# Optimization experiments

Measured on AMD Instinct MI355X. Metric: run time of the kernel, lower is better.

The kernel has to match this reference:

```python
import jax, jax.numpy as jnp
import numpy as np
import math

WINDOW_SIZE = 11
DATA_RANGE = 1.0
SIGMA = 1.5


def _gaussian_window(C):
    xs = np.arange(WINDOW_SIZE)
    g = np.exp(-((xs - WINDOW_SIZE // 2) ** 2) / (2.0 * SIGMA ** 2))
    g = (g / g.sum()).astype(np.float32)
    w2d = np.outer(g, g)  # [K,K]
    # depthwise kernel: [C, 1, K, K] in OIHW with feature_group_count=C
    w = np.broadcast_to(w2d, (C, 1, WINDOW_SIZE, WINDOW_SIZE))
    return jnp.asarray(w)


def _dwconv(x, w, C):
    pad = WINDOW_SIZE // 2
    return jax.lax.conv_general_dilated(
        x, w, window_strides=(1, 1), padding=((pad, pad), (pad, pad)),
        dimension_numbers=('NCHW', 'OIHW', 'NCHW'), feature_group_count=C)


def setup_inputs() -> dict:
    key = jax.random.key(0)
    k1, k2 = jax.random.split(key)
    B, C, H, W = 16, 3, 512, 512
    img1 = jax.random.uniform(k1, (B, C, H, W), dtype=jnp.float32)
    img2 = jax.random.uniform(k2, (B, C, H, W), dtype=jnp.float32)
    return {"img1": img1, "img2": img2}


def reference(img1, img2):
    C = img1.shape[1]
    w = _gaussian_window(C)
    C1 = (0.01 * DATA_RANGE) ** 2
    C2 = (0.03 * DATA_RANGE) ** 2

    mu1 = _dwconv(img1, w, C)
    mu2 = _dwconv(img2, w, C)
    mu1_sq = mu1 * mu1
    mu2_sq = mu2 * mu2
    mu1_mu2 = mu1 * mu2
    sigma1_sq = _dwconv(img1 * img1, w, C) - mu1_sq
    sigma2_sq = _dwconv(img2 * img2, w, C) - mu2_sq
    sigma12 = _dwconv(img1 * img2, w, C) - mu1_mu2

    ssim_map = ((2 * mu1_mu2 + C1) * (2 * sigma12 + C2)) / (
        (mu1_sq + mu2_sq + C1) * (sigma1_sq + sigma2_sq + C2))
    ssim_val = ssim_map.mean(axis=(1, 2, 3)).mean()  # size_average=True
    return 1.0 - ssim_val
```

## Files before the change

kernel.cpp:

```cpp
#include <hip/hip_runtime.h>
#include <math.h>

typedef float v2f __attribute__((ext_vector_type(2)));

#define TILE 32
#define HALO 5
#define IN_T 42
#define ROWP 42
#define SINT_P 33
#define HWDIM 512
#define NPLANES 48
#define NBLK (16*16*48)
#define NPIX (16ull*3ull*512ull*512ull)

struct GW { float g[11]; };

__global__ __launch_bounds__(256) void ssim_reduce(
    const float* __restrict__ partial, float* __restrict__ out)
{
    __shared__ float s_red[4];
    const int tid = threadIdx.x;
    float s = 0.0f;
#pragma unroll
    for (int k = 0; k < NBLK / 256; ++k) s += partial[tid + k * 256];
#pragma unroll
    for (int off = 32; off > 0; off >>= 1) s += __shfl_down(s, off, 64);
    if ((tid & 63) == 0) s_red[tid >> 6] = s;
    __syncthreads();
    if (tid == 0) {
        const float tot = s_red[0] + s_red[1] + s_red[2] + s_red[3];
        out[0] = 1.0f - tot * (1.0f / (float)NPIX);
    }
}

__global__ __launch_bounds__(256, 4) void ssim_main(
    const float* __restrict__ img1, const float* __restrict__ img2,
    float* __restrict__ partial, GW gw)
{
    __shared__ alignas(16) v2f sxy[IN_T][ROWP];
    __shared__ alignas(16) float4 s_int[IN_T][SINT_P];
    __shared__ float s_red[4];

    const int tid = threadIdx.x;
    const int tx = blockIdx.x, ty = blockIdx.y, plane = blockIdx.z;
    const float* __restrict__ p1 = img1 + (size_t)plane * (HWDIM * HWDIM);
    const float* __restrict__ p2 = img2 + (size_t)plane * (HWDIM * HWDIM);
    const int gy0 = ty * TILE - HALO;
    const int gx0 = tx * TILE - HALO;

    for (int idx = tid; idx < IN_T * ROWP; idx += 256) {
        const int r = idx / ROWP;
        const int c = idx - r * ROWP;
        const int gy = gy0 + r, gx = gx0 + c;
        float a = 0.0f, b = 0.0f;
        if (gy >= 0 && gy < HWDIM && gx >= 0 && gx < HWDIM) {
            const int off = gy * HWDIM + gx;
            a = p1[off];
            b = p2[off];
        }
        v2f pr; pr.x = a; pr.y = b;
        sxy[r][c] = pr;
    }
    __syncthreads();

    for (int item = tid; item < IN_T * 8; item += 256) {
        const int g8 = item / IN_T;
        const int r  = item - g8 * IN_T;
        const int c0 = g8 * 4;

        v2f xy[14];
#pragma unroll
        for (int j = 0; j < 7; ++j) {
            const float4 f = *reinterpret_cast<const float4*>(&sxy[r][c0 + 2 * j]);
            v2f t0; t0.x = f.x; t0.y = f.y;
            v2f t1; t1.x = f.z; t1.y = f.w;
            xy[2 * j]     = t0;
            xy[2 * j + 1] = t1;
        }

        v2f accA[4], accB[4];
#pragma unroll
        for (int o = 0; o < 4; ++o) { accA[o] = 0.0f; accB[o] = 0.0f; }

#pragma unroll
        for (int e = 0; e < 14; ++e) {
            const v2f p = xy[e];
            const float u = p.x + p.y;
            const float w = p.x - p.y;
            v2f uv; uv.x = u; uv.y = w;
            const v2f qq = uv * uv;
#pragma unroll
            for (int o = 0; o < 4; ++o) {
                const int k = e - o;
                if (k >= 0 && k < 11) {
                    v2f gg; gg.x = gw.g[k]; gg.y = gw.g[k];
                    accA[o] = __builtin_elementwise_fma(gg, p,  accA[o]);
                    accB[o] = __builtin_elementwise_fma(gg, qq, accB[o]);
                }
            }
        }
#pragma unroll
        for (int o = 0; o < 4; ++o)
            s_int[r][c0 + o] = make_float4(accA[o].x, accA[o].y, accB[o].x, accB[o].y);
    }
    __syncthreads();

    const int c  = tid & 31;
    const int r0 = (tid >> 5) * 4;
    v2f vA[4], vB[4];
#pragma unroll
    for (int o = 0; o < 4; ++o) { vA[o] = 0.0f; vB[o] = 0.0f; }

#pragma unroll
    for (int j = 0; j < 14; ++j) {
        const float4 f = s_int[r0 + j][c];
        v2f A; A.x = f.x; A.y = f.y;
        v2f B; B.x = f.z; B.y = f.w;
#pragma unroll
        for (int o = 0; o < 4; ++o) {
            const int k = j - o;
            if (k >= 0 && k < 11) {
                v2f gg; gg.x = gw.g[k]; gg.y = gw.g[k];
                vA[o] = __builtin_elementwise_fma(gg, A, vA[o]);
                vB[o] = __builtin_elementwise_fma(gg, B, vB[o]);
            }
        }
    }

    const float C1 = 0.01f * 0.01f;
    const float C2 = 0.03f * 0.03f;
    float lsum = 0.0f;
#pragma unroll
    for (int o = 0; o < 4; ++o) {
        const float mu1 = vA[o].x;
        const float mu2 = vA[o].y;
        const float s_uu = vB[o].x;
        const float s_vv = vB[o].y;
        const float mu1_sq = mu1 * mu1;
        const float mu2_sq = mu2 * mu2;
        const float mu1_mu2 = mu1 * mu2;
        const float sigma12 = (s_uu - s_vv) * 0.25f - mu1_mu2;
        const float sigsum  = (s_uu + s_vv) * 0.5f - mu1_sq - mu2_sq;
        const float num = (2.0f * mu1_mu2 + C1) * (2.0f * sigma12 + C2);
        const float den = (mu1_sq + mu2_sq + C1) * (sigsum + C2);
        lsum += num / den;
    }

#pragma unroll
    for (int off = 32; off > 0; off >>= 1) lsum += __shfl_down(lsum, off, 64);
    if ((tid & 63) == 0) s_red[tid >> 6] = lsum;
    __syncthreads();
    if (tid == 0) {
        const int bid = (blockIdx.z * gridDim.y + blockIdx.y) * gridDim.x + blockIdx.x;
        partial[bid] = s_red[0] + s_red[1] + s_red[2] + s_red[3];
    }
}

extern "C" void kernel_launch(void* const* d_in, const int* in_sizes, int n_in,
                              void* d_out, int out_size, void* d_ws, size_t ws_size,
                              hipStream_t stream) {
    const float* img1 = (const float*)d_in[0];
    const float* img2 = (const float*)d_in[1];
    float* out = (float*)d_out;
    float* wsf = (float*)d_ws;

    GW gw;
    {
        double g[11], s = 0.0;
        for (int i = 0; i < 11; ++i) {
            const double d = (double)(i - 5);
            g[i] = exp(-(d * d) / (2.0 * 1.5 * 1.5));
            s += g[i];
        }
        for (int i = 0; i < 11; ++i) gw.g[i] = (float)(g[i] / s);
    }

    dim3 grid(HWDIM / TILE, HWDIM / TILE, NPLANES);
    ssim_main<<<grid, 256, 0, stream>>>(img1, img2, wsf, gw);
    ssim_reduce<<<1, 256, 0, stream>>>(wsf, out);
}
```

Measured before the change: 181.8 us.

## Merge SSIM reduction into persistent cooperative kernel with grid sync

Turns the main kernel into a persistent grid-stride loop over tiles, launched cooperatively with occupancy-sized block count, and performs the final reduction after a grid-wide sync instead of a second kernel launch. Also replaces the division with a fast reciprocal multiply-add. This aims to remove the extra launch and tail effects, but adds host-side device property and occupancy queries on every call plus grid sync overhead, and loses overlap of tile loading across blocks since each block processes tiles serially with syncthreads barriers.

```diff
diff --git a/kernel.cpp b/kernel.cpp
--- a/kernel.cpp
+++ b/kernel.cpp
@@ -1,5 +1,8 @@
 #include <hip/hip_runtime.h>
+#include <hip/hip_cooperative_groups.h>
 #include <math.h>
+
+namespace cg = cooperative_groups;
 
 typedef float v2f __attribute__((ext_vector_type(2)));
 
@@ -10,149 +13,150 @@
 #define SINT_P 33
 #define HWDIM 512
 #define NPLANES 48
-#define NBLK (16*16*48)
+#define NTILES (16*16*48)
 #define NPIX (16ull*3ull*512ull*512ull)
 
 struct GW { float g[11]; };
 
-__global__ __launch_bounds__(256) void ssim_reduce(
-    const float* __restrict__ partial, float* __restrict__ out)
-{
-    __shared__ float s_red[4];
-    const int tid = threadIdx.x;
-    float s = 0.0f;
-#pragma unroll
-    for (int k = 0; k < NBLK / 256; ++k) s += partial[tid + k * 256];
-#pragma unroll
-    for (int off = 32; off > 0; off >>= 1) s += __shfl_down(s, off, 64);
-    if ((tid & 63) == 0) s_red[tid >> 6] = s;
-    __syncthreads();
-    if (tid == 0) {
-        const float tot = s_red[0] + s_red[1] + s_red[2] + s_red[3];
-        out[0] = 1.0f - tot * (1.0f / (float)NPIX);
-    }
-}
-
 __global__ __launch_bounds__(256, 4) void ssim_main(
     const float* __restrict__ img1, const float* __restrict__ img2,
-    float* __restrict__ partial, GW gw)
+    float* __restrict__ partial, float* __restrict__ out, GW gw)
 {
     __shared__ alignas(16) v2f sxy[IN_T][ROWP];
     __shared__ alignas(16) float4 s_int[IN_T][SINT_P];
     __shared__ float s_red[4];
 
     const int tid = threadIdx.x;
-    const int tx = blockIdx.x, ty = blockIdx.y, plane = blockIdx.z;
-    const float* __restrict__ p1 = img1 + (size_t)plane * (HWDIM * HWDIM);
-    const float* __restrict__ p2 = img2 + (size_t)plane * (HWDIM * HWDIM);
-    const int gy0 = ty * TILE - HALO;
-    const int gx0 = tx * TILE - HALO;
+    const float C1 = 0.01f * 0.01f;
+    const float C2 = 0.03f * 0.03f;
+    float lsum = 0.0f;
 
-    for (int idx = tid; idx < IN_T * ROWP; idx += 256) {
-        const int r = idx / ROWP;
-        const int c = idx - r * ROWP;
-        const int gy = gy0 + r, gx = gx0 + c;
-        float a = 0.0f, b = 0.0f;
-        if (gy >= 0 && gy < HWDIM && gx >= 0 && gx < HWDIM) {
-            const int off = gy * HWDIM + gx;
-            a = p1[off];
-            b = p2[off];
+    for (unsigned T = blockIdx.x; T < NTILES; T += gridDim.x) {
+        const unsigned plane = T >> 8;
+        const unsigned rem   = T & 255u;
+        const unsigned ty    = rem >> 4;
+        const unsigned tx    = rem & 15u;
+        const float* __restrict__ p1 = img1 + (size_t)plane * (HWDIM * HWDIM);
+        const float* __restrict__ p2 = img2 + (size_t)plane * (HWDIM * HWDIM);
+        const int gy0 = (int)ty * TILE - HALO;
+        const int gx0 = (int)tx * TILE - HALO;
+
+        for (int idx = tid; idx < IN_T * ROWP; idx += 256) {
+            const int r = idx / ROWP;
+            const int c = idx - r * ROWP;
+            const int gy = gy0 + r, gx = gx0 + c;
+            float a = 0.0f, b = 0.0f;
+            if (gy >= 0 && gy < HWDIM && gx >= 0 && gx < HWDIM) {
+                const int off = gy * HWDIM + gx;
+                a = p1[off];
+                b = p2[off];
+            }
+            v2f pr; pr.x = a; pr.y = b;
+            sxy[r][c] = pr;
         }
-        v2f pr; pr.x = a; pr.y = b;
-        sxy[r][c] = pr;
-    }
-    __syncthreads();
+        __syncthreads();
 
-    for (int item = tid; item < IN_T * 8; item += 256) {
-        const int g8 = item / IN_T;
-        const int r  = item - g8 * IN_T;
-        const int c0 = g8 * 4;
+        for (int item = tid; item < IN_T * 8; item += 256) {
+            const int g8 = item / IN_T;
+            const int r  = item - g8 * IN_T;
+            const int c0 = g8 * 4;
 
-        v2f xy[14];
+            v2f xy[14];
 #pragma unroll
-        for (int j = 0; j < 7; ++j) {
-            const float4 f = *reinterpret_cast<const float4*>(&sxy[r][c0 + 2 * j]);
-            v2f t0; t0.x = f.x; t0.y = f.y;
-            v2f t1; t1.x = f.z; t1.y = f.w;
-            xy[2 * j]     = t0;
-            xy[2 * j + 1] = t1;
-        }
+            for (int j = 0; j < 7; ++j) {
+                const float4 f = *reinterpret_cast<const float4*>(&sxy[r][c0 + 2 * j]);
+                v2f t0; t0.x = f.x; t0.y = f.y;
+                v2f t1; t1.x = f.z; t1.y = f.w;
+                xy[2 * j]     = t0;
+                xy[2 * j + 1] = t1;
+            }
 
-        v2f accA[4], accB[4];
+            v2f accA[4], accB[4];
 #pragma unroll
-        for (int o = 0; o < 4; ++o) { accA[o] = 0.0f; accB[o] = 0.0f; }
+            for (int o = 0; o < 4; ++o) { accA[o] = 0.0f; accB[o] = 0.0f; }
 
 #pragma unroll
-        for (int e = 0; e < 14; ++e) {
-            const v2f p = xy[e];
-            const float u = p.x + p.y;
-            const float w = p.x - p.y;
-            v2f uv; uv.x = u; uv.y = w;
-            const v2f qq = uv * uv;
+            for (int e = 0; e < 14; ++e) {
+                const v2f p = xy[e];
+                const float u = p.x + p.y;
+                const float w = p.x - p.y;
+                v2f uv; uv.x = u; uv.y = w;
+                const v2f qq = uv * uv;
+#pragma unroll
+                for (int o = 0; o < 4; ++o) {
+                    const int k = e - o;
+                    if (k >= 0 && k < 11) {
+                        v2f gg; gg.x = gw.g[k]; gg.y = gw.g[k];
+                        accA[o] = __builtin_elementwise_fma(gg, p,  accA[o]);
+                        accB[o] = __builtin_elementwise_fma(gg, qq, accB[o]);
+                    }
+                }
+            }
+#pragma unroll
+            for (int o = 0; o < 4; ++o)
+                s_int[r][c0 + o] = make_float4(accA[o].x, accA[o].y, accB[o].x, accB[o].y);
+        }
+        __syncthreads();
+
+        const int c  = tid & 31;
+        const int r0 = (tid >> 5) * 4;
+        v2f vA[4], vB[4];
+#pragma unroll
+        for (int o = 0; o < 4; ++o) { vA[o] = 0.0f; vB[o] = 0.0f; }
+
+#pragma unroll
+        for (int j = 0; j < 14; ++j) {
+            const float4 f = s_int[r0 + j][c];
+            v2f A; A.x = f.x; A.y = f.y;
+            v2f B; B.x = f.z; B.y = f.w;
 #pragma unroll
             for (int o = 0; o < 4; ++o) {
-                const int k = e - o;
+                const int k = j - o;
                 if (k >= 0 && k < 11) {
                     v2f gg; gg.x = gw.g[k]; gg.y = gw.g[k];
-                    accA[o] = __builtin_elementwise_fma(gg, p,  accA[o]);
-                    accB[o] = __builtin_elementwise_fma(gg, qq, accB[o]);
+                    vA[o] = __builtin_elementwise_fma(gg, A, vA[o]);
+                    vB[o] = __builtin_elementwise_fma(gg, B, vB[o]);
                 }
             }
         }
-#pragma unroll
-        for (int o = 0; o < 4; ++o)
-            s_int[r][c0 + o] = make_float4(accA[o].x, accA[o].y, accB[o].x, accB[o].y);
-    }
-    __syncthreads();
-
-    const int c  = tid & 31;
-    const int r0 = (tid >> 5) * 4;
-    v2f vA[4], vB[4];
-#pragma unroll
-    for (int o = 0; o < 4; ++o) { vA[o] = 0.0f; vB[o] = 0.0f; }
 
 #pragma unroll
-    for (int j = 0; j < 14; ++j) {
-        const float4 f = s_int[r0 + j][c];
-        v2f A; A.x = f.x; A.y = f.y;
-        v2f B; B.x = f.z; B.y = f.w;
-#pragma unroll
         for (int o = 0; o < 4; ++o) {
-            const int k = j - o;
-            if (k >= 0 && k < 11) {
-                v2f gg; gg.x = gw.g[k]; gg.y = gw.g[k];
-                vA[o] = __builtin_elementwise_fma(gg, A, vA[o]);
-                vB[o] = __builtin_elementwise_fma(gg, B, vB[o]);
-            }
+            const float mu1 = vA[o].x;
+            const float mu2 = vA[o].y;
+            const float s_uu = vB[o].x;
+            const float s_vv = vB[o].y;
+            const float mu1_sq = mu1 * mu1;
+            const float mu2_sq = mu2 * mu2;
+            const float mu1_mu2 = mu1 * mu2;
+            const float sigma12 = (s_uu - s_vv) * 0.25f - mu1_mu2;
+            const float sigsum  = (s_uu + s_vv) * 0.5f - mu1_sq - mu2_sq;
+            const float num = (2.0f * mu1_mu2 + C1) * (2.0f * sigma12 + C2);
+            const float den = (mu1_sq + mu2_sq + C1) * (sigsum + C2);
+            lsum = fmaf(num, __builtin_amdgcn_rcpf(den), lsum);
         }
-    }
-
-    const float C1 = 0.01f * 0.01f;
-    const float C2 = 0.03f * 0.03f;
-    float lsum = 0.0f;
-#pragma unroll
-    for (int o = 0; o < 4; ++o) {
-        const float mu1 = vA[o].x;
-        const float mu2 = vA[o].y;
-        const float s_uu = vB[o].x;
-        const float s_vv = vB[o].y;
-        const float mu1_sq = mu1 * mu1;
-        const float mu2_sq = mu2 * mu2;
-        const float mu1_mu2 = mu1 * mu2;
-        const float sigma12 = (s_uu - s_vv) * 0.25f - mu1_mu2;
-        const float sigsum  = (s_uu + s_vv) * 0.5f - mu1_sq - mu2_sq;
-        const float num = (2.0f * mu1_mu2 + C1) * (2.0f * sigma12 + C2);
-        const float den = (mu1_sq + mu2_sq + C1) * (sigsum + C2);
-        lsum += num / den;
     }
 
 #pragma unroll
     for (int off = 32; off > 0; off >>= 1) lsum += __shfl_down(lsum, off, 64);
     if ((tid & 63) == 0) s_red[tid >> 6] = lsum;
     __syncthreads();
-    if (tid == 0) {
-        const int bid = (blockIdx.z * gridDim.y + blockIdx.y) * gridDim.x + blockIdx.x;
-        partial[bid] = s_red[0] + s_red[1] + s_red[2] + s_red[3];
+    if (tid == 0)
+        partial[blockIdx.x] = s_red[0] + s_red[1] + s_red[2] + s_red[3];
+
+    cg::this_grid().sync();
+
+    if (blockIdx.x == 0) {
+        float s = 0.0f;
+        for (unsigned i = tid; i < gridDim.x; i += 256) s += partial[i];
+#pragma unroll
+        for (int off = 32; off > 0; off >>= 1) s += __shfl_down(s, off, 64);
+        if ((tid & 63) == 0) s_red[tid >> 6] = s;
+        __syncthreads();
+        if (tid == 0) {
+            const float tot = s_red[0] + s_red[1] + s_red[2] + s_red[3];
+            out[0] = 1.0f - tot * (1.0f / (float)NPIX);
+        }
     }
 }
 
@@ -162,7 +166,7 @@
     const float* img1 = (const float*)d_in[0];
     const float* img2 = (const float*)d_in[1];
     float* out = (float*)d_out;
-    float* wsf = (float*)d_ws;
+    float* partial = (float*)d_ws;
 
     GW gw;
     {
@@ -175,7 +179,19 @@
         for (int i = 0; i < 11; ++i) gw.g[i] = (float)(g[i] / s);
     }
 
-    dim3 grid(HWDIM / TILE, HWDIM / TILE, NPLANES);
-    ssim_main<<<grid, 256, 0, stream>>>(img1, img2, wsf, gw);
-    ssim_reduce<<<1, 256, 0, stream>>>(wsf, out);
+    int dev = 0;
+    hipGetDevice(&dev);
+    hipDeviceProp_t prop;
+    hipGetDeviceProperties(&prop, dev);
+    int perCU = 0;
+    hipOccupancyMaxActiveBlocksPerMultiprocessor(&perCU, ssim_main, 256, 0);
+    if (perCU < 1) perCU = 1;
+    if (perCU > 4) perCU = 4;
+    unsigned nblocks = (unsigned)(perCU * prop.multiProcessorCount);
+    if (nblocks > NTILES) nblocks = NTILES;
+
+    void* args[] = { (void*)&img1, (void*)&img2, (void*)&partial,
+                     (void*)&out, (void*)&gw };
+    hipLaunchCooperativeKernel(ssim_main, dim3(nblocks), dim3(256),
+                               args, 0, stream);
 }
```

Measured after the change: 272.7 us. 50.0% more time.
